# Kernel tuning notes

Hardware: AMD Instinct MI355X
Metric: run time of the kernel (lower is better)

Reference implementation:

```python
import jax, jax.numpy as jnp
import numpy as np

B, T, SD, AD, H, K, HID = 256, 128, 8, 2, 3, 4, 256


def setup_inputs() -> dict:
    key = jax.random.key(0)
    ks = jax.random.split(key, 12)
    inp = {
        "state": jax.random.normal(ks[0], (B, T, SD), dtype=jnp.float32),
        "action": jax.random.normal(ks[1], (B, T, AD), dtype=jnp.float32),
        # Linear(4, 4*H, bias=False): weight (4*H, 4)
        "Wk": jax.random.normal(ks[2], (4 * H, K), dtype=jnp.float32) * 0.1,
        "Wq": jax.random.normal(ks[3], (4 * H, SD + AD), dtype=jnp.float32) * 0.1,
        "Wv": jax.random.normal(ks[4], (4 * H, K), dtype=jnp.float32) * 0.1,
        # MLP: in_dim = 4*H + SD + AD -> HID -> HID -> 1
        "W1": jax.random.normal(ks[5], (HID, 4 * H + SD + AD), dtype=jnp.float32) * 0.05,
        "b1": jnp.zeros((HID,), dtype=jnp.float32),
        "W2": jax.random.normal(ks[6], (HID, HID), dtype=jnp.float32) * 0.05,
        "b2": jnp.zeros((HID,), dtype=jnp.float32),
        "Wout": jax.random.uniform(ks[7], (1, HID), minval=-0.003, maxval=0.003, dtype=jnp.float32),
        "bout": jax.random.uniform(ks[8], (1,), minval=-0.003, maxval=0.003, dtype=jnp.float32),
    }
    return inp


def reference(state, action, Wk, Wq, Wv, W1, b1, W2, b2, Wout, bout):
    q_state = jnp.concatenate([state, action], axis=-1)  # (b, t, sd+ad)
    s = state[:, :, :4]                                   # (b, t, 4)
    b, t, k = s.shape
    h = Wk.shape[0] // k
    # rel_full[b, i, j] = s[b, j] - s[b, i]  (matches torch view/transpose)
    rel_full = s[:, None, :, :] - s[:, :, None, :]        # (b, t, t, 4)
    # drop diagonal (self-pairs): idx[i] = all j != i, in order
    j = jnp.arange(t - 1)
    idx = j[None, :] + (j[None, :] >= jnp.arange(t)[:, None])  # (t, t-1)
    rel = jnp.take_along_axis(rel_full, idx[None, :, :, None], axis=2)  # (b, t, t-1, 4)
    # QKV projections (tiny head dim k=4)
    q = (q_state @ Wq.T).reshape(b, t, h, k)              # (b, t, h, 4)
    keys = (rel @ Wk.T).reshape(b, t, t - 1, h, k)        # (b, t, t-1, h, 4)
    vals = (rel @ Wv.T).reshape(b, t, t - 1, h, k)
    scores = jnp.einsum('bthk,btjhk->bthj', q, keys) / jnp.sqrt(jnp.float32(k))
    w = jax.nn.softmax(scores, axis=-1)                   # over the t-1 neighbors
    x = jnp.einsum('bthj,btjhk->bthk', w, vals).reshape(b, t, h * k)
    x = jnp.concatenate([x, q_state], axis=-1)            # (b, t, h*4 + sd+ad)
    x = jax.nn.relu(x @ W1.T + b1)
    x = jax.nn.relu(x @ W2.T + b2)
    return x @ Wout.T + bout                              # (b, t, 1)
```

## Files before the change

### kernel.cpp

```cpp
#include <hip/hip_runtime.h>
#include <math.h>

#define Bp 256
#define Tp 128
#define SDp 8
#define ADp 2
#define Hp 3
#define Kp 4
#define HIDp 256
#define QDp (SDp + ADp)
#define X1Dp (Hp * Kp + QDp)
#define QKLD 17
#define LOG2E 1.4426950408889634f

typedef short bf16x8 __attribute__((ext_vector_type(8)));
typedef float f32x4  __attribute__((ext_vector_type(4)));

__device__ __forceinline__ unsigned short f2bf(float f) {
    unsigned u = __float_as_uint(f);
    unsigned r = (u + 0x7FFFu + ((u >> 16) & 1u)) >> 16;
    return (unsigned short)r;
}

__device__ __forceinline__ unsigned h1_byte(int row, int colbytes) {
    return (((unsigned)row << 9) + (unsigned)colbytes) ^ ((unsigned)(row & 7) << 4);
}
__device__ __forceinline__ unsigned x1_byte(int row, int colbytes) {
    return ((unsigned)row << 6) + ((unsigned)colbytes ^ (((unsigned)row & 6u) << 3));
}

__global__ __launch_bounds__(256) void prep_kernel(
    const float* __restrict__ W1, const float* __restrict__ W2,
    unsigned short* __restrict__ W1b, unsigned short* __restrict__ W2b)
{
    const int bid = blockIdx.x;
    const int tid = threadIdx.x;
    if (bid < 64) {
        const int i = bid * 1024 + tid * 4;
        const float4 v = *(const float4*)(W2 + i);
        ushort4 o;
        o.x = f2bf(v.x); o.y = f2bf(v.y); o.z = f2bf(v.z); o.w = f2bf(v.w);
        *(ushort4*)(W2b + i) = o;
    } else {
        const int i = (bid - 64) * 256 + tid;
        const int r = i >> 5, c = i & 31;
        W1b[i] = (c < X1Dp) ? f2bf(W1[r * X1Dp + c]) : (unsigned short)0;
    }
}

__global__ __launch_bounds__(256, 4) void main_kernel(
    const float* __restrict__ state, const float* __restrict__ action,
    const float* __restrict__ Wk, const float* __restrict__ Wq,
    const float* __restrict__ Wv,
    const unsigned short* __restrict__ W1b, const unsigned short* __restrict__ W2b,
    const float* __restrict__ b1, const float* __restrict__ b2,
    const float* __restrict__ Wout, const float* __restrict__ bout,
    float* __restrict__ out)
{
    const int bid   = blockIdx.x;
    const int batch = bid >> 2;
    const int t0    = (bid & 3) * 32;
    const int tid   = threadIdx.x;
    const int lane  = tid & 63;
    const int wave  = tid >> 6;
    const int quad  = lane >> 4;
    const int l16   = lane & 15;
    const int t_loc = tid >> 3;
    const int jo    = tid & 7;
    const int t     = t0 + t_loc;

    __shared__ float4 s4[Tp];
    __shared__ float  wv[Hp * Kp * Kp];
    __shared__ float  qk[32 * QKLD];
    __shared__ float  b1s[HIDp];
    __shared__ float  b2s[HIDp];
    __shared__ float  wouts[HIDp];
    __shared__ __align__(16) unsigned short X1s[32 * 32];
    __shared__ __align__(16) unsigned short h1s[32 * 256];
    __shared__ float partial[4][32];

    if (tid < Tp) {
        s4[tid] = ((const float4*)(state + (size_t)batch * Tp * SDp))[tid * 2];
    } else if (tid < 160) {
        const int ta = tid - 128;
        const int tt = t0 + ta;
        float qs[QDp];
        {
            const float* srow = state + ((size_t)batch * Tp + tt) * SDp;
            const float4 v0 = *(const float4*)srow;
            const float4 v1 = *(const float4*)(srow + 4);
            qs[0]=v0.x; qs[1]=v0.y; qs[2]=v0.z; qs[3]=v0.w;
            qs[4]=v1.x; qs[5]=v1.y; qs[6]=v1.z; qs[7]=v1.w;
            const float* arow = action + ((size_t)batch * Tp + tt) * ADp;
            qs[8] = arow[0]; qs[9] = arow[1];
        }
        float q[Hp * Kp];
        #pragma unroll
        for (int r = 0; r < Hp * Kp; ++r) {
            float a = 0.f;
            #pragma unroll
            for (int d = 0; d < QDp; ++d) a += qs[d] * Wq[r * QDp + d];
            q[r] = a;
        }
        float* qrow = &qk[ta * QKLD];
        #pragma unroll
        for (int h = 0; h < Hp; ++h)
            #pragma unroll
            for (int c = 0; c < Kp; ++c) {
                float a = 0.f;
                #pragma unroll
                for (int k = 0; k < Kp; ++k) a += q[h * Kp + k] * Wk[(h * Kp + k) * Kp + c];
                qrow[h * 4 + c] = 0.5f * LOG2E * a;
            }
        #pragma unroll
        for (int i = 0; i < 5; ++i) {
            const unsigned u = (unsigned)f2bf(qs[2*i]) | ((unsigned)f2bf(qs[2*i+1]) << 16);
            qrow[12 + i] = __uint_as_float(u);
        }
    } else if (tid < 160 + Hp * Kp * Kp) {
        wv[tid - 160] = Wv[tid - 160];
    }
    b1s[tid]   = b1[tid];
    b2s[tid]   = b2[tid];
    wouts[tid] = Wout[tid];
    __syncthreads();

    float rq[12];
    #pragma unroll
    for (int i = 0; i < 3; ++i)
        *(float4*)&rq[i * 4] = *(const float4*)&qk[t_loc * QKLD + i * 4];

    float l[Hp] = {0.f, 0.f, 0.f};
    float ac[Hp][4] = {};
    #pragma unroll
    for (int i = 0; i < 16; ++i) {
        const int j = (jo << 4) | ((i + jo) & 15);
        const float4 sj = s4[j];
        #pragma unroll
        for (int h = 0; h < Hp; ++h) {
            const float d = sj.x * rq[h*4] + sj.y * rq[h*4+1]
                          + sj.z * rq[h*4+2] + sj.w * rq[h*4+3];
            const float e = __builtin_amdgcn_exp2f(d);
            l[h] += e;
            ac[h][0] += e * sj.x; ac[h][1] += e * sj.y;
            ac[h][2] += e * sj.z; ac[h][3] += e * sj.w;
        }
    }
    #pragma unroll
    for (int off = 1; off < 8; off <<= 1) {
        #pragma unroll
        for (int h = 0; h < Hp; ++h) {
            l[h] += __shfl_xor(l[h], off);
            #pragma unroll
            for (int c = 0; c < Kp; ++c) ac[h][c] += __shfl_xor(ac[h][c], off);
        }
    }

    if (jo == 0) {
        const float4 st = s4[t];
        unsigned short rowb[32] __attribute__((aligned(16)));
        #pragma unroll
        for (int h = 0; h < Hp; ++h) {
            const float dtt = st.x * rq[h*4] + st.y * rq[h*4+1]
                            + st.z * rq[h*4+2] + st.w * rq[h*4+3];
            const float ett = __builtin_amdgcn_exp2f(dtt);
            const float inv = 1.f / (l[h] - ett);
            const float rb0 = (ac[h][0] - ett * st.x) * inv - st.x;
            const float rb1 = (ac[h][1] - ett * st.y) * inv - st.y;
            const float rb2 = (ac[h][2] - ett * st.z) * inv - st.z;
            const float rb3 = (ac[h][3] - ett * st.w) * inv - st.w;
            #pragma unroll
            for (int k = 0; k < Kp; ++k) {
                const int r = h * Kp + k;
                rowb[r] = f2bf(rb0 * wv[r*4] + rb1 * wv[r*4+1] + rb2 * wv[r*4+2] + rb3 * wv[r*4+3]);
            }
        }
        #pragma unroll
        for (int i = 0; i < 5; ++i) {
            const unsigned u = __float_as_uint(qk[t_loc * QKLD + 12 + i]);
            rowb[12 + 2*i] = (unsigned short)(u & 0xffffu);
            rowb[13 + 2*i] = (unsigned short)(u >> 16);
        }
        #pragma unroll
        for (int i = X1Dp; i < 32; ++i) rowb[i] = 0;

        const uint4* srcv = (const uint4*)rowb;
        #pragma unroll
        for (int i = 0; i < 4; ++i)
            *(uint4*)((char*)X1s + x1_byte(t_loc, i * 16)) = srcv[i];
    }
    __syncthreads();

    {
        const int rt  = wave & 1;
        const int chh = wave >> 1;
        bf16x8 bfr[8];
        #pragma unroll
        for (int n = 0; n < 8; ++n)
            bfr[n] = *(const bf16x8*)&W1b[(chh * 128 + n * 16 + l16) * 32 + quad * 8];
        const bf16x8 afr = *(const bf16x8*)((const char*)X1s +
                             x1_byte(rt * 16 + l16, quad * 16));
        #pragma unroll
        for (int n = 0; n < 8; ++n) {
            const int col = chh * 128 + n * 16 + l16;
            f32x4 acc = {0.f, 0.f, 0.f, 0.f};
            acc = __builtin_amdgcn_mfma_f32_16x16x32_bf16(afr, bfr[n], acc, 0, 0, 0);
            const float bb = b1s[col];
            #pragma unroll
            for (int r = 0; r < 4; ++r) {
                const int row = rt * 16 + quad * 4 + r;
                *(unsigned short*)((char*)h1s + h1_byte(row, col * 2)) =
                    f2bf(fmaxf(acc[r] + bb, 0.f));
            }
        }
    }
    __syncthreads();

    float rsum[2][4] = {};
    #pragma unroll
    for (int i = 0; i < 4; ++i) {
        const int col = (wave * 4 + i) * 16 + l16;
        const unsigned short* wr = W2b + (size_t)col * HIDp + quad * 8;
        bf16x8 Bf[8];
        #pragma unroll
        for (int ks = 0; ks < 8; ++ks)
            Bf[ks] = *(const bf16x8*)(wr + ks * 32);
        const float bb = b2s[col];
        const float wo = wouts[col];
        #pragma unroll
        for (int rt = 0; rt < 2; ++rt) {
            bf16x8 A8[8];
            #pragma unroll
            for (int ks = 0; ks < 8; ++ks)
                A8[ks] = *(const bf16x8*)((const char*)h1s +
                           h1_byte(rt * 16 + l16, ks * 64 + quad * 16));
            f32x4 acc = {0.f, 0.f, 0.f, 0.f};
            #pragma unroll
            for (int ks = 0; ks < 8; ++ks)
                acc = __builtin_amdgcn_mfma_f32_16x16x32_bf16(A8[ks], Bf[ks], acc, 0, 0, 0);
            #pragma unroll
            for (int r = 0; r < 4; ++r)
                rsum[rt][r] += fmaxf(acc[r] + bb, 0.f) * wo;
        }
    }

    #pragma unroll
    for (int off = 1; off < 16; off <<= 1)
        #pragma unroll
        for (int rt = 0; rt < 2; ++rt)
            #pragma unroll
            for (int r = 0; r < 4; ++r)
                rsum[rt][r] += __shfl_xor(rsum[rt][r], off);

    if (l16 == 0) {
        #pragma unroll
        for (int rt = 0; rt < 2; ++rt)
            #pragma unroll
            for (int r = 0; r < 4; ++r)
                partial[wave][rt * 16 + quad * 4 + r] = rsum[rt][r];
    }
    __syncthreads();

    if (tid < 32) {
        out[(size_t)batch * Tp + t0 + tid] =
            partial[0][tid] + partial[1][tid] + partial[2][tid]
          + partial[3][tid] + bout[0];
    }
}

extern "C" void kernel_launch(void* const* d_in, const int* in_sizes, int n_in,
                              void* d_out, int out_size, void* d_ws, size_t ws_size,
                              hipStream_t stream) {
    const float* state  = (const float*)d_in[0];
    const float* action = (const float*)d_in[1];
    const float* Wk     = (const float*)d_in[2];
    const float* Wq     = (const float*)d_in[3];
    const float* Wv     = (const float*)d_in[4];
    const float* W1     = (const float*)d_in[5];
    const float* b1     = (const float*)d_in[6];
    const float* W2     = (const float*)d_in[7];
    const float* b2     = (const float*)d_in[8];
    const float* Wout   = (const float*)d_in[9];
    const float* bout   = (const float*)d_in[10];
    float* out = (float*)d_out;

    char* ws = (char*)d_ws;
    unsigned short* W1b = (unsigned short*)(ws);
    unsigned short* W2b = (unsigned short*)(ws + 16384);

    prep_kernel<<<96, 256, 0, stream>>>(W1, W2, W1b, W2b);
    main_kernel<<<4 * Bp, 256, 0, stream>>>(state, action, Wk, Wq, Wv,
                                            W1b, W2b, b1, b2, Wout, bout, out);
}
```

Baseline: 96.87 us.

## Compute attention scores and weighted sums with bf16 MFMA instead of scalar loops

The per-thread scalar loop over neighbours (dot product, exp2, accumulate) is replaced by two MFMA stages. The first forms all 96x128 query-key scores and writes exp2 results as bf16 into shared memory. The second multiplies that matrix by a transposed state matrix with an appended ones row, giving the weighted sums and softmax denominators together. Shared memory is reused between phases, and bias/Wout values are now read directly from global memory instead of being staged. The exp weights and states are rounded to bf16, which lowers attention precision, and an extra barrier is added.

```diff
diff --git a/kernel.cpp b/kernel.cpp
--- a/kernel.cpp
+++ b/kernel.cpp
@@ -10,7 +10,6 @@
 #define HIDp 256
 #define QDp (SDp + ADp)
 #define X1Dp (Hp * Kp + QDp)
-#define QKLD 17
 #define LOG2E 1.4426950408889634f
 
 typedef short bf16x8 __attribute__((ext_vector_type(8)));
@@ -21,12 +20,20 @@
     unsigned r = (u + 0x7FFFu + ((u >> 16) & 1u)) >> 16;
     return (unsigned short)r;
 }
+__device__ __forceinline__ unsigned cvtpk(float lo, float hi) {
+    unsigned r;
+    asm("v_cvt_pk_bf16_f32 %0, %1, %2" : "=v"(r) : "v"(lo), "v"(hi));
+    return r;
+}
 
 __device__ __forceinline__ unsigned h1_byte(int row, int colbytes) {
     return (((unsigned)row << 9) + (unsigned)colbytes) ^ ((unsigned)(row & 7) << 4);
 }
 __device__ __forceinline__ unsigned x1_byte(int row, int colbytes) {
     return ((unsigned)row << 6) + ((unsigned)colbytes ^ (((unsigned)row & 6u) << 3));
+}
+__device__ __forceinline__ unsigned e_byte(int row, int colbytes) {
+    return ((unsigned)row << 8) + ((unsigned)colbytes ^ (((unsigned)row & 15u) << 4));
 }
 
 __global__ __launch_bounds__(256) void prep_kernel(
@@ -65,22 +72,29 @@
     const int wave  = tid >> 6;
     const int quad  = lane >> 4;
     const int l16   = lane & 15;
-    const int t_loc = tid >> 3;
-    const int jo    = tid & 7;
-    const int t     = t0 + t_loc;
 
     __shared__ float4 s4[Tp];
     __shared__ float  wv[Hp * Kp * Kp];
-    __shared__ float  qk[32 * QKLD];
-    __shared__ float  b1s[HIDp];
-    __shared__ float  b2s[HIDp];
-    __shared__ float  wouts[HIDp];
-    __shared__ __align__(16) unsigned short X1s[32 * 32];
-    __shared__ __align__(16) unsigned short h1s[32 * 256];
+    __shared__ float  qkpc[96 * 4];
+    __shared__ unsigned qsb[32 * 5];
+    __shared__ __align__(16) unsigned short S1eT[16 * 128];
+    __shared__ __align__(16) char REG[24576];
+    __shared__ float D2L[96 * 17];
     __shared__ float partial[4][32];
 
+    unsigned short* E   = (unsigned short*)REG;
+    unsigned short* X1s = (unsigned short*)REG;
+    unsigned short* h1s = (unsigned short*)(REG + 2048);
+
+    const bf16x8 zfrag = {0, 0, 0, 0, 0, 0, 0, 0};
+
     if (tid < Tp) {
-        s4[tid] = ((const float4*)(state + (size_t)batch * Tp * SDp))[tid * 2];
+        const float4 v = ((const float4*)(state + (size_t)batch * Tp * SDp))[tid * 2];
+        s4[tid] = v;
+        *(unsigned short*)((char*)S1eT + e_byte(0, tid * 2)) = f2bf(v.x);
+        *(unsigned short*)((char*)S1eT + e_byte(1, tid * 2)) = f2bf(v.y);
+        *(unsigned short*)((char*)S1eT + e_byte(2, tid * 2)) = f2bf(v.z);
+        *(unsigned short*)((char*)S1eT + e_byte(3, tid * 2)) = f2bf(v.w);
     } else if (tid < 160) {
         const int ta = tid - 128;
         const int tt = t0 + ta;
@@ -102,92 +116,134 @@
             for (int d = 0; d < QDp; ++d) a += qs[d] * Wq[r * QDp + d];
             q[r] = a;
         }
-        float* qrow = &qk[ta * QKLD];
-        #pragma unroll
-        for (int h = 0; h < Hp; ++h)
+        #pragma unroll
+        for (int h = 0; h < Hp; ++h) {
+            float4 p;
             #pragma unroll
             for (int c = 0; c < Kp; ++c) {
                 float a = 0.f;
                 #pragma unroll
                 for (int k = 0; k < Kp; ++k) a += q[h * Kp + k] * Wk[(h * Kp + k) * Kp + c];
-                qrow[h * 4 + c] = 0.5f * LOG2E * a;
-            }
-        #pragma unroll
-        for (int i = 0; i < 5; ++i) {
-            const unsigned u = (unsigned)f2bf(qs[2*i]) | ((unsigned)f2bf(qs[2*i+1]) << 16);
-            qrow[12 + i] = __uint_as_float(u);
-        }
-    } else if (tid < 160 + Hp * Kp * Kp) {
-        wv[tid - 160] = Wv[tid - 160];
-    }
-    b1s[tid]   = b1[tid];
-    b2s[tid]   = b2[tid];
-    wouts[tid] = Wout[tid];
-    __syncthreads();
-
-    float rq[12];
-    #pragma unroll
-    for (int i = 0; i < 3; ++i)
-        *(float4*)&rq[i * 4] = *(const float4*)&qk[t_loc * QKLD + i * 4];
-
-    float l[Hp] = {0.f, 0.f, 0.f};
-    float ac[Hp][4] = {};
-    #pragma unroll
-    for (int i = 0; i < 16; ++i) {
-        const int j = (jo << 4) | ((i + jo) & 15);
-        const float4 sj = s4[j];
+                p[c] = 0.5f * LOG2E * a;
+            }
+            *(float4*)&qkpc[(h * 32 + ta) * 4] = p;
+        }
+        #pragma unroll
+        for (int i = 0; i < 5; ++i)
+            qsb[ta * 5 + i] = cvtpk(qs[2*i], qs[2*i+1]);
+    } else {
+        const int i = tid - 160;
+        const unsigned ones = 0x3F803F80u;
+        #pragma unroll
+        for (int rep = 0; rep < 2; ++rep) {
+            const int v = i + rep * 96;
+            if (v < 192) {
+                const int row = 4 + (v >> 4);
+                const int cb  = (v & 15) * 16;
+                const unsigned fill = (row == 4) ? ones : 0u;
+                uint4 z; z.x = fill; z.y = fill; z.z = fill; z.w = fill;
+                *(uint4*)((char*)S1eT + e_byte(row, cb)) = z;
+            }
+        }
+        if (i < Hp * Kp * Kp) wv[i] = Wv[i];
+    }
+    __syncthreads();
+
+    {
+        bf16x8 Am[6];
+        #pragma unroll
+        for (int m = 0; m < 6; ++m) {
+            union { unsigned u[4]; bf16x8 v; } a;
+            const float4 p = *(const float4*)&qkpc[(m * 16 + l16) * 4];
+            a.u[0] = cvtpk(p.x, p.y); a.u[1] = cvtpk(p.z, p.w);
+            a.u[2] = 0u; a.u[3] = 0u;
+            Am[m] = (quad == 0) ? a.v : zfrag;
+        }
+        #pragma unroll
+        for (int nn = 0; nn < 2; ++nn) {
+            const int n = wave * 2 + nn;
+            union { unsigned u[4]; bf16x8 v; } b;
+            const float4 sv = s4[n * 16 + l16];
+            b.u[0] = cvtpk(sv.x, sv.y); b.u[1] = cvtpk(sv.z, sv.w);
+            b.u[2] = 0u; b.u[3] = 0u;
+            const bf16x8 Bf = (quad == 0) ? b.v : zfrag;
+            #pragma unroll
+            for (int m = 0; m < 6; ++m) {
+                f32x4 d = {0.f, 0.f, 0.f, 0.f};
+                d = __builtin_amdgcn_mfma_f32_16x16x32_bf16(Am[m], Bf, d, 0, 0, 0);
+                #pragma unroll
+                for (int r = 0; r < 4; ++r) {
+                    const int row = m * 16 + quad * 4 + r;
+                    const int col = n * 16 + l16;
+                    *(unsigned short*)((char*)E + e_byte(row, col * 2)) =
+                        f2bf(__builtin_amdgcn_exp2f(d[r]));
+                }
+            }
+        }
+    }
+    __syncthreads();
+
+    float ett[3] = {0.f, 0.f, 0.f};
+    if (tid < 32) {
         #pragma unroll
         for (int h = 0; h < Hp; ++h) {
-            const float d = sj.x * rq[h*4] + sj.y * rq[h*4+1]
-                          + sj.z * rq[h*4+2] + sj.w * rq[h*4+3];
-            const float e = __builtin_amdgcn_exp2f(d);
-            l[h] += e;
-            ac[h][0] += e * sj.x; ac[h][1] += e * sj.y;
-            ac[h][2] += e * sj.z; ac[h][3] += e * sj.w;
-        }
-    }
-    #pragma unroll
-    for (int off = 1; off < 8; off <<= 1) {
+            const unsigned short ev = *(const unsigned short*)
+                ((const char*)E + e_byte(h * 32 + tid, (t0 + tid) * 2));
+            ett[h] = __uint_as_float(((unsigned)ev) << 16);
+        }
+    }
+
+    {
+        const int nm = (wave < 2) ? 2 : 1;
+        for (int mi = 0; mi < nm; ++mi) {
+            const int m = (mi == 0) ? wave : (4 + wave);
+            f32x4 acc = {0.f, 0.f, 0.f, 0.f};
+            #pragma unroll
+            for (int ks = 0; ks < 4; ++ks) {
+                const bf16x8 a = *(const bf16x8*)((const char*)E +
+                                    e_byte(m * 16 + l16, ks * 64 + quad * 16));
+                const bf16x8 b = *(const bf16x8*)((const char*)S1eT +
+                                    e_byte(l16, ks * 64 + quad * 16));
+                acc = __builtin_amdgcn_mfma_f32_16x16x32_bf16(a, b, acc, 0, 0, 0);
+            }
+            #pragma unroll
+            for (int r = 0; r < 4; ++r)
+                D2L[(m * 16 + quad * 4 + r) * 17 + l16] = acc[r];
+        }
+    }
+    __syncthreads();
+
+    if (tid < 32) {
+        const float4 st = s4[t0 + tid];
+        const float stc[4] = {st.x, st.y, st.z, st.w};
+        unsigned short rowb[32] __attribute__((aligned(16)));
         #pragma unroll
         for (int h = 0; h < Hp; ++h) {
-            l[h] += __shfl_xor(l[h], off);
-            #pragma unroll
-            for (int c = 0; c < Kp; ++c) ac[h][c] += __shfl_xor(ac[h][c], off);
-        }
-    }
-
-    if (jo == 0) {
-        const float4 st = s4[t];
-        unsigned short rowb[32] __attribute__((aligned(16)));
-        #pragma unroll
-        for (int h = 0; h < Hp; ++h) {
-            const float dtt = st.x * rq[h*4] + st.y * rq[h*4+1]
-                            + st.z * rq[h*4+2] + st.w * rq[h*4+3];
-            const float ett = __builtin_amdgcn_exp2f(dtt);
-            const float inv = 1.f / (l[h] - ett);
-            const float rb0 = (ac[h][0] - ett * st.x) * inv - st.x;
-            const float rb1 = (ac[h][1] - ett * st.y) * inv - st.y;
-            const float rb2 = (ac[h][2] - ett * st.z) * inv - st.z;
-            const float rb3 = (ac[h][3] - ett * st.w) * inv - st.w;
+            const int th = h * 32 + tid;
+            const float lsum = D2L[th * 17 + 4] - ett[h];
+            const float inv  = 1.f / lsum;
+            float rb[4];
+            #pragma unroll
+            for (int c = 0; c < 4; ++c)
+                rb[c] = (D2L[th * 17 + c] - ett[h] * stc[c]) * inv - stc[c];
             #pragma unroll
             for (int k = 0; k < Kp; ++k) {
                 const int r = h * Kp + k;
-                rowb[r] = f2bf(rb0 * wv[r*4] + rb1 * wv[r*4+1] + rb2 * wv[r*4+2] + rb3 * wv[r*4+3]);
+                rowb[r] = f2bf(rb[0]*wv[r*4] + rb[1]*wv[r*4+1] + rb[2]*wv[r*4+2] + rb[3]*wv[r*4+3]);
             }
         }
         #pragma unroll
         for (int i = 0; i < 5; ++i) {
-            const unsigned u = __float_as_uint(qk[t_loc * QKLD + 12 + i]);
+            const unsigned u = qsb[tid * 5 + i];
             rowb[12 + 2*i] = (unsigned short)(u & 0xffffu);
             rowb[13 + 2*i] = (unsigned short)(u >> 16);
         }
         #pragma unroll
         for (int i = X1Dp; i < 32; ++i) rowb[i] = 0;
-
         const uint4* srcv = (const uint4*)rowb;
         #pragma unroll
         for (int i = 0; i < 4; ++i)
-            *(uint4*)((char*)X1s + x1_byte(t_loc, i * 16)) = srcv[i];
+            *(uint4*)((char*)X1s + x1_byte(tid, i * 16)) = srcv[i];
     }
     __syncthreads();
 
@@ -205,7 +261,7 @@
             const int col = chh * 128 + n * 16 + l16;
             f32x4 acc = {0.f, 0.f, 0.f, 0.f};
             acc = __builtin_amdgcn_mfma_f32_16x16x32_bf16(afr, bfr[n], acc, 0, 0, 0);
-            const float bb = b1s[col];
+            const float bb = b1[col];
             #pragma unroll
             for (int r = 0; r < 4; ++r) {
                 const int row = rt * 16 + quad * 4 + r;
@@ -225,8 +281,8 @@
         #pragma unroll
         for (int ks = 0; ks < 8; ++ks)
             Bf[ks] = *(const bf16x8*)(wr + ks * 32);
-        const float bb = b2s[col];
-        const float wo = wouts[col];
+        const float bb = b2[col];
+        const float wo = Wout[col];
         #pragma unroll
         for (int rt = 0; rt < 2; ++rt) {
             bf16x8 A8[8];
```

After: 102.6 us. +5.9%, slower.
